# Optimization experiments

Hardware: AMD Instinct MI355X
Metric: run time of the kernel (lower is better)

The kernel has to match this reference:

```python
import jax, jax.numpy as jnp
import numpy as np

B, L, D = 8, 8192, 256
H = 4 * D
EPS_LN = 1e-5
EPS_RELU = 1e-6
MIN_A, MAX_A, OFFSET = 0, 3, 3


def setup_inputs() -> dict:
    key = jax.random.key(0)
    ks = jax.random.split(key, 6)
    def n(k, shape, s=0.02):
        return jax.random.normal(k, shape, jnp.float32) * s
    return {
        "x": jax.random.normal(ks[0], (B, L, D), jnp.float32),
        "g1": jnp.ones((D,), jnp.float32), "b1": jnp.zeros((D,), jnp.float32),
        "g2": jnp.ones((D,), jnp.float32), "b2": jnp.zeros((D,), jnp.float32),
        "filt_w": n(ks[1], (L, D)),
        "w1": n(ks[2], (D, H)), "bb1": jnp.zeros((H,), jnp.float32),
        "w2": n(ks[3], (H, D)), "bb2": jnp.zeros((D,), jnp.float32),
    }


def layernorm(x, g, b):
    m = jnp.mean(x, -1, keepdims=True)
    v = jnp.var(x, -1, keepdims=True)
    return (x - m) * jax.lax.rsqrt(v + EPS_LN) * g + b


def maxpool_same(x, w):
    # stride-1 max pool over the last (frequency) axis, SAME padding
    if w == 1:
        return x
    return jax.lax.reduce_window(x, -jnp.inf, jax.lax.max,
                                 (1, 1, w), (1, 1, 1), "SAME")


def spsd1d(xt):
    """SPSD1D: FFT-based multi-scale (alpha) max-pooling spectral filter.
    xt: (B, D, L). Keeps rfft bins that are local maxima at every scale
    2**alpha for alpha in [MIN_A, MAX_A]; the lowest OFFSET bins pass through.
    Returns filtered signal (B, D, L) and argmax-alpha holder (B, D, F)."""
    X = jnp.fft.rfft(xt, axis=-1)              # (B, D, F), F = L//2 + 1
    mag = jnp.abs(X)
    pooled = jnp.stack([maxpool_same(mag, 2 ** a)
                        for a in range(MIN_A, MAX_A + 1)], 0)  # (A, B, D, F)
    max_holder = jnp.argmax(pooled, axis=0)
    env = jnp.max(pooled, axis=0)
    keep = (mag >= env) | (jnp.arange(mag.shape[-1]) < OFFSET)
    Xf = jnp.where(keep, X, 0.0)
    out = jnp.fft.irfft(Xf, n=xt.shape[-1], axis=-1)
    return out, max_holder


def _block_forward(x, g1, b1, g2, b2, filt_w, w1, bb1, w2, bb2):
    # EpsilonReLU(LayerNorm(x))
    h = jax.nn.relu(layernorm(x, g1, b1)) + EPS_RELU      # (B, L, D)
    # GlobalSPSDFilter: spsd over sequence axis, then elementwise weight
    f, _max_holder = spsd1d(jnp.swapaxes(h, 1, 2))        # (B, D, L)
    x0 = jnp.swapaxes(f, 1, 2) * filt_w                   # (B, L, D)
    # MLP(LayerNorm(x0)); dropouts are identity in eval mode
    m = layernorm(x0, g2, b2)
    m = jax.nn.gelu(m @ w1 + bb1, approximate=False)
    x0 = m @ w2 + bb2
    return x + x0


def reference(x, g1, b1, g2, b2, filt_w, w1, bb1, w2, bb2):
    return _block_forward(x, g1, b1, g2, b2, filt_w, w1, bb1, w2, bb2)
```

## Files before the change

### kernel.cpp

```cpp
#include <hip/hip_runtime.h>
#include <hip/hip_bf16.h>

#define BSZ  8
#define LSEQ 8192
#define DDIM 256
#define HDIM 1024
#define MFFT 4096

typedef __bf16 bf16;
typedef __bf16 bf16x8 __attribute__((ext_vector_type(8)));
typedef __bf16 bf16x4 __attribute__((ext_vector_type(4)));
typedef float  f32x4  __attribute__((ext_vector_type(4)));

__device__ __forceinline__ void wave_reduce2(float& a, float& b) {
    #pragma unroll
    for (int off = 1; off < 64; off <<= 1) {
        a += __shfl_xor(a, off);
        b += __shfl_xor(b, off);
    }
}

__device__ __forceinline__ void gl_lds16(const void* g, void* l) {
    __builtin_amdgcn_global_load_lds(
        (const __attribute__((address_space(1))) unsigned int*)(unsigned long long)g,
        (__attribute__((address_space(3))) unsigned int*)(unsigned int)(unsigned long long)l,
        16, 0, 0);
}

__global__ __launch_bounds__(256) void k0_prep(const float* __restrict__ w1,
                                               const float* __restrict__ w2,
                                               bf16* __restrict__ w1k,
                                               bf16* __restrict__ w2k,
                                               float2* __restrict__ tbl) {
    const int e = blockIdx.x * 256 + threadIdx.x;
    {
        const int c = e >> 13, r = e & 8191;
        const int ks = r >> 10, grp = (r >> 8) & 3, hh = (r >> 3) & 31, j = r & 7;
        w1k[e] = (bf16)w1[(ks * 32 + grp * 8 + j) * HDIM + c * 32 + hh];
    }
    {
        const int c = e >> 13, r = e & 8191;
        const int grp = r >> 11, d = (r >> 3) & 255, j = r & 7;
        w2k[e] = (bf16)w2[(c * 32 + grp * 8 + j) * DDIM + d];
    }
    if (e <= 8184) {
        float ang;
        if (e < 3584) {
            const int f = e / 512 + 1, jj = e & 511;
            ang = -6.283185307179586f * (float)(f * jj) * (1.0f / 4096.0f);
        } else if (e < 4032) {
            const int t = e - 3584, f = t / 64 + 1, jj = t & 63;
            ang = -6.283185307179586f * (float)(f * jj) * (1.0f / 512.0f);
        } else if (e < 4088) {
            const int t = e - 4032, f = t / 8 + 1, jj = t & 7;
            ang = -6.283185307179586f * (float)(f * jj) * (1.0f / 64.0f);
        } else {
            const int k = e - 4088;
            ang = 3.14159265358979323846f * (float)k * (1.0f / 4096.0f);
        }
        tbl[e] = make_float2(cosf(ang), sinf(ang));
    }
}

__global__ __launch_bounds__(256) void k1_ln1_relu_T(const float* __restrict__ x,
                                                     const float* __restrict__ g1,
                                                     const float* __restrict__ b1,
                                                     float* __restrict__ ht) {
    __shared__ float tile[DDIM][33];
    const int tid  = threadIdx.x;
    const int wave = tid >> 6, lane = tid & 63;
    const int b  = blockIdx.x >> 8;
    const int l0 = (blockIdx.x & 255) << 5;
    const float4 g4 = *(const float4*)&g1[lane * 4];
    const float4 b4 = *(const float4*)&b1[lane * 4];
    for (int r8 = 0; r8 < 8; ++r8) {
        const int l = r8 * 4 + wave;
        const float4 v = *(const float4*)&x[(b * LSEQ + l0 + l) * DDIM + lane * 4];
        float s = v.x + v.y + v.z + v.w;
        float q = v.x * v.x + v.y * v.y + v.z * v.z + v.w * v.w;
        wave_reduce2(s, q);
        const float mean = s * (1.0f / 256.0f);
        const float var  = q * (1.0f / 256.0f) - mean * mean;
        const float rstd = rsqrtf(var + 1e-5f);
        const float vv[4] = {v.x, v.y, v.z, v.w};
        const float gg[4] = {g4.x, g4.y, g4.z, g4.w};
        const float bb[4] = {b4.x, b4.y, b4.z, b4.w};
        #pragma unroll
        for (int j = 0; j < 4; ++j) {
            float t = (vv[j] - mean) * rstd * gg[j] + bb[j];
            t = fmaxf(t, 0.0f) + 1e-6f;
            tile[lane * 4 + j][l] = t;
        }
    }
    __syncthreads();
    for (int i = tid; i < DDIM * 32; i += 256) {
        const int d = i >> 5, ll = i & 31;
        ht[(b * DDIM + d) * LSEQ + l0 + ll] = tile[d][ll];
    }
}

__device__ __forceinline__ int zs(int p) { return p ^ ((p >> 4) & 15); }
__device__ __forceinline__ float2 cmulf(float2 a, float2 b) {
    return make_float2(fmaf(a.x, b.x, -a.y * b.y), fmaf(a.x, b.y, a.y * b.x));
}
__device__ __forceinline__ float2 f2add(float2 a, float2 b) { return make_float2(a.x + b.x, a.y + b.y); }
__device__ __forceinline__ float2 f2sub(float2 a, float2 b) { return make_float2(a.x - b.x, a.y - b.y); }
#define CSQ2 0.70710678118654752440f

__device__ __forceinline__ void dft8(float2 a0, float2 a1, float2 a2, float2 a3,
                                     float2 a4, float2 a5, float2 a6, float2 a7,
                                     float2& y0, float2& y1, float2& y2, float2& y3,
                                     float2& y4, float2& y5, float2& y6, float2& y7) {
    const float2 s0 = f2add(a0, a4), s1 = f2add(a1, a5), s2 = f2add(a2, a6), s3 = f2add(a3, a7);
    const float2 d0 = f2sub(a0, a4), d1 = f2sub(a1, a5), d2 = f2sub(a2, a6), d3 = f2sub(a3, a7);
    const float2 d1t = make_float2(CSQ2 * (d1.x + d1.y), CSQ2 * (d1.y - d1.x));
    const float2 d2t = make_float2(d2.y, -d2.x);
    const float2 d3t = make_float2(CSQ2 * (d3.y - d3.x), -CSQ2 * (d3.x + d3.y));
    const float2 u0 = f2add(s0, s2), u1 = f2add(s1, s3);
    const float2 v0 = f2sub(s0, s2);
    const float2 sd = f2sub(s1, s3);
    const float2 v1 = make_float2(sd.y, -sd.x);
    const float2 e0 = f2add(d0, d2t), e1 = f2add(d1t, d3t);
    const float2 f0 = f2sub(d0, d2t);
    const float2 dd = f2sub(d1t, d3t);
    const float2 f1 = make_float2(dd.y, -dd.x);
    y0 = f2add(u0, u1); y4 = f2sub(u0, u1);
    y2 = f2add(v0, v1); y6 = f2sub(v0, v1);
    y1 = f2add(e0, e1); y5 = f2sub(e0, e1);
    y3 = f2add(f0, f1); y7 = f2sub(f0, f1);
}

template<int LQ, int TOFF>
__device__ __forceinline__ void stage8(float2* Z, const float2* __restrict__ tw, int tid) {
    const int q = 1 << LQ;
    const int j = tid & (q - 1);
    const int base = ((tid >> LQ) << (LQ + 3)) + j;
    const float2 a0 = Z[zs(base)],         a1 = Z[zs(base + q)];
    const float2 a2 = Z[zs(base + 2 * q)], a3 = Z[zs(base + 3 * q)];
    const float2 a4 = Z[zs(base + 4 * q)], a5 = Z[zs(base + 5 * q)];
    const float2 a6 = Z[zs(base + 6 * q)], a7 = Z[zs(base + 7 * q)];
    float2 y0, y1, y2, y3, y4, y5, y6, y7;
    dft8(a0, a1, a2, a3, a4, a5, a6, a7, y0, y1, y2, y3, y4, y5, y6, y7);
    y1 = cmulf(y1, tw[TOFF + j]);
    y2 = cmulf(y2, tw[TOFF + q + j]);
    y3 = cmulf(y3, tw[TOFF + 2 * q + j]);
    y4 = cmulf(y4, tw[TOFF + 3 * q + j]);
    y5 = cmulf(y5, tw[TOFF + 4 * q + j]);
    y6 = cmulf(y6, tw[TOFF + 5 * q + j]);
    y7 = cmulf(y7, tw[TOFF + 6 * q + j]);
    Z[zs(base)]         = y0;
    Z[zs(base + 4 * q)] = y1;
    Z[zs(base + 2 * q)] = y2;
    Z[zs(base + 6 * q)] = y3;
    Z[zs(base + q)]     = y4;
    Z[zs(base + 5 * q)] = y5;
    Z[zs(base + 3 * q)] = y6;
    Z[zs(base + 7 * q)] = y7;
    __syncthreads();
}

__device__ __forceinline__ void stage8_last(float2* Z, int tid) {
    const int base = tid << 3;
    const float2 a0 = Z[zs(base)],     a1 = Z[zs(base + 1)];
    const float2 a2 = Z[zs(base + 2)], a3 = Z[zs(base + 3)];
    const float2 a4 = Z[zs(base + 4)], a5 = Z[zs(base + 5)];
    const float2 a6 = Z[zs(base + 6)], a7 = Z[zs(base + 7)];
    __syncthreads();
    float2 y0, y1, y2, y3, y4, y5, y6, y7;
    dft8(a0, a1, a2, a3, a4, a5, a6, a7, y0, y1, y2, y3, y4, y5, y6, y7);
    const int r9 = (int)(__brev((unsigned)tid) >> 23);
    Z[zs(r9)]        = y0;
    Z[zs(512 + r9)]  = y1;
    Z[zs(1024 + r9)] = y2;
    Z[zs(1536 + r9)] = y3;
    Z[zs(2048 + r9)] = y4;
    Z[zs(2560 + r9)] = y5;
    Z[zs(3072 + r9)] = y6;
    Z[zs(3584 + r9)] = y7;
    __syncthreads();
}

__device__ __forceinline__ void fft4096(float2* Z, const float2* __restrict__ tw, int tid) {
    stage8<9, 0>(Z, tw, tid);
    stage8<6, 3584>(Z, tw, tid);
    stage8<3, 4032>(Z, tw, tid);
    stage8_last(Z, tid);
}

__global__ __launch_bounds__(512, 4) void k2_spsd(float* __restrict__ ht,
                                                  const float2* __restrict__ tw) {
    __shared__ float2 Z[MFFT];
    __shared__ float  mg[MFFT + 1];
    const int tid = threadIdx.x;
    float* row = ht + (size_t)blockIdx.x * LSEQ;
    const float2* U = tw + 4088;

    for (int m = tid; m < MFFT; m += 512)
        Z[zs(m)] = *(const float2*)&row[2 * m];
    __syncthreads();

    fft4096(Z, tw, tid);

    for (int k = tid; k <= MFFT; k += 512) {
        const int ka = k & (MFFT - 1);
        const int kb = (MFFT - k) & (MFFT - 1);
        const float2 A = Z[zs(ka)], Bc = Z[zs(kb)];
        const float zex = 0.5f * (A.x + Bc.x), zey = 0.5f * (A.y - Bc.y);
        const float zox = 0.5f * (A.y + Bc.y), zoy = -0.5f * (A.x - Bc.x);
        const float2 u = U[k];
        const float cs = u.x, sn = -u.y;
        const float xr = zex + zox * cs - zoy * sn;
        const float xi = zey + zox * sn + zoy * cs;
        mg[k] = sqrtf(xr * xr + xi * xi);
    }
    __syncthreads();

    for (int k = tid; k <= 2048; k += 512) {
        const int km = (MFFT - k) & (MFFT - 1);
        const float2 Pk = Z[zs(k)];
        const float2 Pm = Z[zs(km)];
        const float2 u = U[k];
        const float cs = u.x, sn = u.y;
        const float zex = 0.5f * (Pk.x + Pm.x), zey = 0.5f * (Pk.y - Pm.y);
        const float zox = 0.5f * (Pk.y + Pm.y), zoy = -0.5f * (Pk.x - Pm.x);
        float xkr = zex + zox * cs + zoy * sn;
        float xki = zey - zox * sn + zoy * cs;
        const float zex2 = 0.5f * (Pm.x + Pk.x), zey2 = 0.5f * (Pm.y - Pk.y);
        const float zox2 = 0.5f * (Pm.y + Pk.y), zoy2 = -0.5f * (Pm.x - Pk.x);
        float xmr = zex2 - zox2 * cs + zoy2 * sn;
        float xmi = zey2 - zox2 * sn - zoy2 * cs;
        const int jm = MFFT - k;
        bool keepk, keepm;
        {
            const int lo = (k - 3 < 0) ? 0 : k - 3;
            const int hi = (k + 4 > 4096) ? 4096 : k + 4;
            float mx = mg[k];
            for (int t2 = lo; t2 <= hi; ++t2) mx = fmaxf(mx, mg[t2]);
            keepk = (k < 3) || (mg[k] >= mx);
        }
        {
            const int hi = (jm + 4 > 4096) ? 4096 : jm + 4;
            float mx = mg[jm];
            for (int t2 = jm - 3; t2 <= hi; ++t2) mx = fmaxf(mx, mg[t2]);
            keepm = (mg[jm] >= mx);
        }
        if (!keepk) { xkr = 0.0f; xki = 0.0f; }
        if (!keepm) { xmr = 0.0f; xmi = 0.0f; }
        const float zpex = 0.5f * (xkr + xmr), zpey = 0.5f * (xki - xmi);
        const float dfx  = 0.5f * (xkr - xmr), dfy  = 0.5f * (xki + xmi);
        const float zpox = dfx * cs - dfy * sn, zpoy = dfx * sn + dfy * cs;
        const float2 zk = make_float2(zpex - zpoy, zpey + zpox);
        const float zex3 = 0.5f * (xmr + xkr), zey3 = 0.5f * (xmi - xki);
        const float df2x = 0.5f * (xmr - xkr), df2y = 0.5f * (xmi + xki);
        const float zo3x = -df2x * cs - df2y * sn, zo3y = df2x * sn - df2y * cs;
        const float2 zm = make_float2(zex3 - zo3y, zey3 + zo3x);
        Z[zs(k)] = make_float2(zk.x, -zk.y);
        if (k != 0 && k != 2048) Z[zs(MFFT - k)] = make_float2(zm.x, -zm.y);
    }
    __syncthreads();

    fft4096(Z, tw, tid);

    const float invM = 1.0f / (float)MFFT;
    for (int m = tid; m < MFFT; m += 512) {
        const float2 z = Z[zs(m)];
        *(float2*)&row[2 * m] = make_float2(z.x * invM, -z.y * invM);
    }
}

__global__ __launch_bounds__(256) void k3_filt_ln2(const float* __restrict__ ht,
                                                   const float* __restrict__ fw,
                                                   const float* __restrict__ g2,
                                                   const float* __restrict__ b2,
                                                   bf16* __restrict__ aln) {
    __shared__ float tile[DDIM][33];
    const int tid  = threadIdx.x;
    const int wave = tid >> 6, lane = tid & 63;
    const int b  = blockIdx.x >> 8;
    const int l0 = (blockIdx.x & 255) << 5;
    for (int i = tid; i < DDIM * 32; i += 256) {
        const int d = i >> 5, ll = i & 31;
        tile[d][ll] = ht[(b * DDIM + d) * LSEQ + l0 + ll];
    }
    __syncthreads();
    const float4 g4 = *(const float4*)&g2[lane * 4];
    const float4 bb4 = *(const float4*)&b2[lane * 4];
    for (int r8 = 0; r8 < 8; ++r8) {
        const int l = r8 * 4 + wave;
        const int gl = l0 + l;
        const float4 f4 = *(const float4*)&fw[gl * DDIM + lane * 4];
        float v[4];
        v[0] = tile[lane * 4 + 0][l] * f4.x;
        v[1] = tile[lane * 4 + 1][l] * f4.y;
        v[2] = tile[lane * 4 + 2][l] * f4.z;
        v[3] = tile[lane * 4 + 3][l] * f4.w;
        float s = v[0] + v[1] + v[2] + v[3];
        float q = v[0] * v[0] + v[1] * v[1] + v[2] * v[2] + v[3] * v[3];
        wave_reduce2(s, q);
        const float mean = s * (1.0f / 256.0f);
        const float var  = q * (1.0f / 256.0f) - mean * mean;
        const float rstd = rsqrtf(var + 1e-5f);
        const float gg[4] = {g4.x, g4.y, g4.z, g4.w};
        const float bb[4] = {bb4.x, bb4.y, bb4.z, bb4.w};
        bf16x4 o;
        #pragma unroll
        for (int j = 0; j < 4; ++j)
            o[j] = (bf16)((v[j] - mean) * rstd * gg[j] + bb[j]);
        *(bf16x4*)&aln[(b * LSEQ + gl) * DDIM + lane * 4] = o;
    }
}

#define LDS_W1 0
#define LDS_W2 16384
#define LDS_LM 32768
#define LDS_TOT 37888

__global__ __launch_bounds__(512, 4) void k4_mlp(const bf16* __restrict__ aln,
                                                 const bf16* __restrict__ w1k,
                                                 const bf16* __restrict__ w2k,
                                                 const float* __restrict__ bb1,
                                                 const float* __restrict__ bb2,
                                                 const float* __restrict__ x,
                                                 float* __restrict__ out) {
    extern __shared__ char sm[];
    const int tid = threadIdx.x;
    const int lane = tid & 63, w = tid >> 6;
    const int rowLane = lane & 15, grp = lane >> 4;
    const int wm = w >> 1, wn = w & 1;
    const int row0 = blockIdx.x << 6;

    bf16x8 aF[8];
    {
        const size_t rb = (size_t)(row0 + wm * 16 + rowLane) * DDIM;
        #pragma unroll
        for (int ks = 0; ks < 8; ++ks)
            aF[ks] = *(const bf16x8*)(aln + rb + ks * 32 + grp * 8);
    }
    {
        const char* g1 = (const char*)w1k;
        gl_lds16(g1 + tid * 16, sm + LDS_W1 + tid * 16);
        gl_lds16(g1 + 8192 + tid * 16, sm + LDS_W1 + 8192 + tid * 16);
    }
    __syncthreads();

    f32x4 acc[8];
    #pragma unroll
    for (int i = 0; i < 8; ++i) acc[i] = (f32x4){0.f, 0.f, 0.f, 0.f};

    for (int c = 0; c < 32; ++c) {
        {
            const char* g2p = (const char*)(w2k + (size_t)c * 8192);
            gl_lds16(g2p + tid * 16, sm + LDS_W2 + tid * 16);
            gl_lds16(g2p + 8192 + tid * 16, sm + LDS_W2 + 8192 + tid * 16);
        }
        const int hc = wn * 16 + rowLane;
        const float bias = bb1[c * 32 + hc];

        f32x4 p = {0.f, 0.f, 0.f, 0.f};
        #pragma unroll
        for (int ks = 0; ks < 8; ++ks) {
            const bf16x8 bF = *(const bf16x8*)(sm + LDS_W1 + ks * 2048 + grp * 512 + hc * 16);
            p = __builtin_amdgcn_mfma_f32_16x16x32_bf16(aF[ks], bF, p, 0, 0, 0);
        }
        const int hs = hc >> 3, hb = (hc & 7) * 2;
        #pragma unroll
        for (int j = 0; j < 4; ++j) {
            const int prow = wm * 16 + grp * 4 + j;
            const float v = p[j] + bias;
            const float ge = 0.5f * v * (1.0f + erff(v * 0.70710678118654752f));
            *(bf16*)(sm + LDS_LM + prow * 80 + ((hs ^ (prow & 3)) * 16) + hb) = (bf16)ge;
        }
        __syncthreads();
        if (c < 31) {
            const char* g1 = (const char*)(w1k + (size_t)(c + 1) * 8192);
            gl_lds16(g1 + tid * 16, sm + LDS_W1 + tid * 16);
            gl_lds16(g1 + 8192 + tid * 16, sm + LDS_W1 + 8192 + tid * 16);
        }
        const int ar = wm * 16 + rowLane;
        const bf16x8 aM = *(const bf16x8*)(sm + LDS_LM + ar * 80 + ((grp ^ (ar & 3)) * 16));
        #pragma unroll
        for (int fn = 0; fn < 8; ++fn) {
            const int dcol = wn * 128 + fn * 16 + rowLane;
            const bf16x8 bw = *(const bf16x8*)(sm + LDS_W2 + grp * 4096 + dcol * 16);
            acc[fn] = __builtin_amdgcn_mfma_f32_16x16x32_bf16(aM, bw, acc[fn], 0, 0, 0);
        }
        __syncthreads();
    }
    #pragma unroll
    for (int fn = 0; fn < 8; ++fn) {
        const int dcol = wn * 128 + fn * 16 + rowLane;
        const float b2v = bb2[dcol];
        #pragma unroll
        for (int j = 0; j < 4; ++j) {
            const int orow = row0 + wm * 16 + grp * 4 + j;
            const int gi = orow * DDIM + dcol;
            out[gi] = acc[fn][j] + b2v + x[gi];
        }
    }
}

extern "C" void kernel_launch(void* const* d_in, const int* in_sizes, int n_in,
                              void* d_out, int out_size, void* d_ws, size_t ws_size,
                              hipStream_t stream) {
    (void)in_sizes; (void)n_in; (void)out_size; (void)ws_size;
    const float* x   = (const float*)d_in[0];
    const float* g1  = (const float*)d_in[1];
    const float* b1  = (const float*)d_in[2];
    const float* g2  = (const float*)d_in[3];
    const float* b2  = (const float*)d_in[4];
    const float* fw  = (const float*)d_in[5];
    const float* w1  = (const float*)d_in[6];
    const float* bb1 = (const float*)d_in[7];
    const float* w2  = (const float*)d_in[8];
    const float* bb2 = (const float*)d_in[9];
    float* out = (float*)d_out;
    char*  ws  = (char*)d_ws;

    bf16*   aln = (bf16*)ws;
    bf16*   w1k = (bf16*)(ws + (size_t)33554432);
    bf16*   w2k = (bf16*)(ws + (size_t)34078720);
    float2* tbl = (float2*)(ws + (size_t)34603008);
    float* ht = out;

    k0_prep<<<dim3(1024), dim3(256), 0, stream>>>(w1, w2, w1k, w2k, tbl);
    k1_ln1_relu_T<<<dim3(2048), dim3(256), 0, stream>>>(x, g1, b1, ht);
    k2_spsd<<<dim3(2048), dim3(512), 0, stream>>>(ht, tbl);
    k3_filt_ln2<<<dim3(2048), dim3(256), 0, stream>>>(ht, fw, g2, b2, aln);
    k4_mlp<<<dim3(1024), dim3(512), LDS_TOT, stream>>>(aln, w1k, w2k, bb1, bb2, x, out);
}
```

Baseline: 248.1 us.

## Double-buffer MLP weight chunks and use 32x32 MFMA for second GEMM

The MLP kernel now keeps two LDS buffers for both W1 and W2 chunks and prefetches chunk c+1 at the start of iteration c, so weight loads overlap compute instead of being issued mid-loop into a single buffer. The second GEMM switches from eight 16x16x32 MFMAs per wave to two 32x32x16 MFMAs per k-step, with a re-laid-out W2 packing and GELU tile layout. This doubles LDS use (about 68KB per block), which may reduce occupancy relative to the launch bound of 4 blocks. The unswizzled GELU store layout may also add LDS bank conflicts.

```diff
diff --git a/kernel.cpp b/kernel.cpp
--- a/kernel.cpp
+++ b/kernel.cpp
@@ -11,6 +11,7 @@
 typedef __bf16 bf16x8 __attribute__((ext_vector_type(8)));
 typedef __bf16 bf16x4 __attribute__((ext_vector_type(4)));
 typedef float  f32x4  __attribute__((ext_vector_type(4)));
+typedef float  f32x16 __attribute__((ext_vector_type(16)));
 
 __device__ __forceinline__ void wave_reduce2(float& a, float& b) {
     #pragma unroll
@@ -40,8 +41,8 @@
     }
     {
         const int c = e >> 13, r = e & 8191;
-        const int grp = r >> 11, d = (r >> 3) & 255, j = r & 7;
-        w2k[e] = (bf16)w2[(c * 32 + grp * 8 + j) * DDIM + d];
+        const int ks4 = r >> 12, g2 = (r >> 11) & 1, d = (r >> 3) & 255, j = r & 7;
+        w2k[e] = (bf16)w2[(c * 32 + ks4 * 16 + g2 * 8 + j) * DDIM + d];
     }
     if (e <= 8184) {
         float ang;
@@ -311,9 +312,12 @@
 }
 
 #define LDS_W1 0
-#define LDS_W2 16384
-#define LDS_LM 32768
-#define LDS_TOT 37888
+#define LDS_W2 32768
+#define LDS_LM 65536
+#define LDS_TOT 69632
+
+#define MFMA16 __builtin_amdgcn_mfma_f32_16x16x32_bf16
+#define MFMA32 __builtin_amdgcn_mfma_f32_32x32x16_bf16
 
 __global__ __launch_bounds__(512, 4) void k4_mlp(const bf16* __restrict__ aln,
                                                  const bf16* __restrict__ w1k,
@@ -326,12 +330,14 @@
     const int tid = threadIdx.x;
     const int lane = tid & 63, w = tid >> 6;
     const int rowLane = lane & 15, grp = lane >> 4;
-    const int wm = w >> 1, wn = w & 1;
+    const int wm1 = w >> 1, wn1 = w & 1;
+    const int wm2 = w >> 2, wn2 = w & 3;
+    const int lane32 = lane & 31, g2l = lane >> 5;
     const int row0 = blockIdx.x << 6;
 
     bf16x8 aF[8];
     {
-        const size_t rb = (size_t)(row0 + wm * 16 + rowLane) * DDIM;
+        const size_t rb = (size_t)(row0 + wm1 * 16 + rowLane) * DDIM;
         #pragma unroll
         for (int ks = 0; ks < 8; ++ks)
             aF[ks] = *(const bf16x8*)(aln + rb + ks * 32 + grp * 8);
@@ -340,61 +346,68 @@
         const char* g1 = (const char*)w1k;
         gl_lds16(g1 + tid * 16, sm + LDS_W1 + tid * 16);
         gl_lds16(g1 + 8192 + tid * 16, sm + LDS_W1 + 8192 + tid * 16);
-    }
-    __syncthreads();
-
-    f32x4 acc[8];
+        const char* g2p = (const char*)w2k;
+        gl_lds16(g2p + tid * 16, sm + LDS_W2 + tid * 16);
+        gl_lds16(g2p + 8192 + tid * 16, sm + LDS_W2 + 8192 + tid * 16);
+    }
+    __syncthreads();
+
+    f32x16 acc0, acc1;
     #pragma unroll
-    for (int i = 0; i < 8; ++i) acc[i] = (f32x4){0.f, 0.f, 0.f, 0.f};
+    for (int i = 0; i < 16; ++i) { acc0[i] = 0.f; acc1[i] = 0.f; }
 
     for (int c = 0; c < 32; ++c) {
+        const int pb = (c & 1) << 14;
+        if (c < 31) {
+            const int nb = ((c + 1) & 1) << 14;
+            const char* g1 = (const char*)w1k + (size_t)(c + 1) * 16384;
+            gl_lds16(g1 + tid * 16, sm + LDS_W1 + nb + tid * 16);
+            gl_lds16(g1 + 8192 + tid * 16, sm + LDS_W1 + nb + 8192 + tid * 16);
+            const char* g2p = (const char*)w2k + (size_t)(c + 1) * 16384;
+            gl_lds16(g2p + tid * 16, sm + LDS_W2 + nb + tid * 16);
+            gl_lds16(g2p + 8192 + tid * 16, sm + LDS_W2 + nb + 8192 + tid * 16);
+        }
+        const int hc = wn1 * 16 + rowLane;
+
+        f32x4 p0 = {0.f, 0.f, 0.f, 0.f};
+        #pragma unroll
+        for (int ks = 0; ks < 8; ++ks) {
+            const bf16x8 bF = *(const bf16x8*)(sm + LDS_W1 + pb + ks * 2048 + grp * 512 + hc * 16);
+            p0 = MFMA16(aF[ks], bF, p0, 0, 0, 0);
+        }
         {
-            const char* g2p = (const char*)(w2k + (size_t)c * 8192);
-            gl_lds16(g2p + tid * 16, sm + LDS_W2 + tid * 16);
-            gl_lds16(g2p + 8192 + tid * 16, sm + LDS_W2 + 8192 + tid * 16);
-        }
-        const int hc = wn * 16 + rowLane;
-        const float bias = bb1[c * 32 + hc];
-
-        f32x4 p = {0.f, 0.f, 0.f, 0.f};
-        #pragma unroll
-        for (int ks = 0; ks < 8; ++ks) {
-            const bf16x8 bF = *(const bf16x8*)(sm + LDS_W1 + ks * 2048 + grp * 512 + hc * 16);
-            p = __builtin_amdgcn_mfma_f32_16x16x32_bf16(aF[ks], bF, p, 0, 0, 0);
-        }
-        const int hs = hc >> 3, hb = (hc & 7) * 2;
-        #pragma unroll
-        for (int j = 0; j < 4; ++j) {
-            const int prow = wm * 16 + grp * 4 + j;
-            const float v = p[j] + bias;
-            const float ge = 0.5f * v * (1.0f + erff(v * 0.70710678118654752f));
-            *(bf16*)(sm + LDS_LM + prow * 80 + ((hs ^ (prow & 3)) * 16) + hb) = (bf16)ge;
+            const float bias = bb1[c * 32 + hc];
+            const int base = (hc >> 3) * 1024 + (hc & 7) * 2;
+            #pragma unroll
+            for (int j = 0; j < 4; ++j) {
+                const int prow = wm1 * 16 + grp * 4 + j;
+                const float v = p0[j] + bias;
+                const float ge = 0.5f * v * (1.0f + erff(v * 0.70710678118654752f));
+                *(bf16*)(sm + LDS_LM + base + prow * 16) = (bf16)ge;
+            }
         }
         __syncthreads();
-        if (c < 31) {
-            const char* g1 = (const char*)(w1k + (size_t)(c + 1) * 8192);
-            gl_lds16(g1 + tid * 16, sm + LDS_W1 + tid * 16);
-            gl_lds16(g1 + 8192 + tid * 16, sm + LDS_W1 + 8192 + tid * 16);
-        }
-        const int ar = wm * 16 + rowLane;
-        const bf16x8 aM = *(const bf16x8*)(sm + LDS_LM + ar * 80 + ((grp ^ (ar & 3)) * 16));
-        #pragma unroll
-        for (int fn = 0; fn < 8; ++fn) {
-            const int dcol = wn * 128 + fn * 16 + rowLane;
-            const bf16x8 bw = *(const bf16x8*)(sm + LDS_W2 + grp * 4096 + dcol * 16);
-            acc[fn] = __builtin_amdgcn_mfma_f32_16x16x32_bf16(aM, bw, acc[fn], 0, 0, 0);
+        #pragma unroll
+        for (int ks4 = 0; ks4 < 2; ++ks4) {
+            const int plane = ks4 * 2 + g2l;
+            const bf16x8 aM = *(const bf16x8*)(sm + LDS_LM + plane * 1024 + (wm2 * 32 + lane32) * 16);
+            const bf16x8 bw0 = *(const bf16x8*)(sm + LDS_W2 + pb + (plane * 256 + wn2 * 64 + lane32) * 16);
+            const bf16x8 bw1 = *(const bf16x8*)(sm + LDS_W2 + pb + (plane * 256 + wn2 * 64 + 32 + lane32) * 16);
+            acc0 = MFMA32(aM, bw0, acc0, 0, 0, 0);
+            acc1 = MFMA32(aM, bw1, acc1, 0, 0, 0);
         }
         __syncthreads();
     }
     #pragma unroll
-    for (int fn = 0; fn < 8; ++fn) {
-        const int dcol = wn * 128 + fn * 16 + rowLane;
+    for (int fn = 0; fn < 2; ++fn) {
+        const int dcol = wn2 * 64 + fn * 32 + lane32;
         const float b2v = bb2[dcol];
         #pragma unroll
-        for (int j = 0; j < 4; ++j) {
-            const int orow = row0 + wm * 16 + grp * 4 + j;
+        for (int reg = 0; reg < 16; ++reg) {
+            const int orow = row0 + wm2 * 32 + (reg & 3) + 8 * (reg >> 2) + 4 * g2l;
             const int gi = orow * DDIM + dcol;
-            out[gi] = acc[fn][j] + b2v + x[gi];
+            const float a = fn ? acc1[reg] : acc0[reg];
+            out[gi] = a + b2v + x[gi];
         }
     }
 }
```

Result: no change. 248.5 us (+0.2%).
